# Kernel tuning notes

Hardware: AMD Instinct MI355X
Metric: run time of the kernel (lower is better)

## Reference

```python
import jax, jax.numpy as jnp
import numpy as np

GROUP = 128  # per-group quantization along the input dimension


def _quantize_int4(w):
    """Asymmetric INT4 per-group quantization. w: [out, in] -> (q, scale, zero).
    q: int32 in [0,15], shape [out, in//GROUP, GROUP]; scale/zero: [out, in//GROUP]."""
    o, i = w.shape
    wg = w.reshape(o, i // GROUP, GROUP)
    mn = wg.min(axis=-1)
    mx = wg.max(axis=-1)
    scale = (mx - mn) / 15.0
    scale = jnp.where(scale == 0, jnp.float32(1.0), scale)
    zero = jnp.clip(jnp.round(-mn / scale), 0.0, 15.0)
    q = jnp.clip(jnp.round(wg / scale[..., None]) + zero[..., None], 0.0, 15.0).astype(jnp.int32)
    return q, scale.astype(jnp.float32), zero.astype(jnp.float32)


def _dequant(q, s, z):
    """(q - zero) * scale, regrouped back to [out, in]."""
    w = (q.astype(jnp.float32) - z[..., None]) * s[..., None]
    return w.reshape(q.shape[0], -1)


def setup_inputs() -> dict:
    key = jax.random.key(0)
    ks = jax.random.split(key, 5)
    B, D_IN, D_H, D_OUT = 512, 2048, 8192, 2048
    x = jax.random.normal(ks[0], (B, D_IN), dtype=jnp.float32)
    w1 = jax.random.normal(ks[1], (D_H, D_IN), dtype=jnp.float32) * 0.02
    b1 = jax.random.normal(ks[2], (D_H,), dtype=jnp.float32) * 0.01
    w2 = jax.random.normal(ks[3], (D_OUT, D_H), dtype=jnp.float32) * 0.02
    b2 = jax.random.normal(ks[4], (D_OUT,), dtype=jnp.float32) * 0.01
    q1, s1, z1 = _quantize_int4(w1)
    q2, s2, z2 = _quantize_int4(w2)
    return {"x": x, "q1": q1, "s1": s1, "z1": z1, "b1": b1,
            "q2": q2, "s2": s2, "z2": z2, "b2": b2}


def reference(x, q1, s1, z1, b1, q2, s2, z2, b2):
    # Layer 1: INT4 dequant + Linear + ReLU (fused in the native kernel)
    w1 = _dequant(q1, s1, z1)              # [D_H, D_IN]
    h = jax.nn.relu(x @ w1.T + b1)         # [B, D_H]
    # Layer 2: INT4 dequant + Linear (no activation)
    w2 = _dequant(q2, s2, z2)              # [D_OUT, D_H]
    return h @ w2.T + b2                   # [B, D_OUT]
```

## Files before the change

kernel.cpp:

```cpp
#include <hip/hip_runtime.h>
#include <stdint.h>

typedef unsigned short u16;
typedef _Float16 f16;
typedef __attribute__((ext_vector_type(8))) _Float16 f16x8;
typedef __attribute__((ext_vector_type(4))) float f32x4;
typedef __attribute__((ext_vector_type(4))) int i32x4;

#define LW 56
#define LWI 28

#define BARRIER() asm volatile("s_waitcnt lgkmcnt(0)\n\ts_barrier" ::: "memory")

__device__ __forceinline__ int pk2(float a, float b) {
  return __builtin_bit_cast(int, __builtin_amdgcn_cvt_pkrtz(a, b));
}


__global__ __launch_bounds__(256) void cvt_x(const float* __restrict__ src,
                                             i32x4* __restrict__ dst, int n8) {
  int t = blockIdx.x * 256 + threadIdx.x;
  if (t >= n8) return;
  f32x4 a = ((const f32x4*)src)[2 * t];
  f32x4 b = ((const f32x4*)src)[2 * t + 1];
  i32x4 o = {pk2(a[0], a[1]), pk2(a[2], a[3]), pk2(b[0], b[1]), pk2(b[2], b[3])};
  dst[t] = o;
}

__global__ __launch_bounds__(256) void bias_init(float* __restrict__ out,
                                                 const float* __restrict__ b, int n4) {
  int t = blockIdx.x * 256 + threadIdx.x;
  if (t >= n4) return;
  int idx = t * 4;
  *(f32x4*)(out + idx) = *(const f32x4*)(b + (idx & 2047));
}

__global__ __launch_bounds__(256, 2) void gemm1(const u16* __restrict__ X,
                                                const int* __restrict__ Q,
                                                const float* __restrict__ S,
                                                const float* __restrict__ Z,
                                                const float* __restrict__ bias,
                                                f16* __restrict__ H) {
  const int K = 2048, N = 8192, G = 16;
  __shared__ int As[2][64 * LWI];
  __shared__ int Bs[2][128 * LWI];
  const int tid = threadIdx.x;
  const int wave = tid >> 6, lane = tid & 63, quad = lane >> 4, l15 = lane & 15;
  const int m0 = blockIdx.y << 6, n0 = blockIdx.x << 7;
  const int wm = (wave >> 1) << 5, wn = (wave & 1) << 6;
  const int arow = tid >> 2, ak = (tid & 3) << 3;
  const int brow = tid >> 1, bk = (tid & 1) << 4;

  const u16* ap = X + (size_t)(m0 + arow) * K + ak;
  const int* qp = Q + (size_t)(n0 + brow) * K + bk;
  const float* sp = S + (n0 + brow) * G;
  const float* zp = Z + (n0 + brow) * G;

  i32x4 nq0 = *(const i32x4*)(qp);
  i32x4 nq1 = *(const i32x4*)(qp + 4);
  i32x4 nq2 = *(const i32x4*)(qp + 8);
  i32x4 nq3 = *(const i32x4*)(qp + 12);
  i32x4 na = *(const i32x4*)(ap);
  float ns = sp[0], nz = zp[0];

  f32x4 acc[2][4];
#pragma unroll
  for (int i = 0; i < 2; i++)
#pragma unroll
    for (int j = 0; j < 4; j++) acc[i][j] = (f32x4){0.f, 0.f, 0.f, 0.f};

#pragma unroll 2
  for (int k = 0; k < K; k += 32) {
    const int buf = (k >> 5) & 1;
    i32x4 q0 = nq0, q1 = nq1, q2 = nq2, q3 = nq3, av = na;
    const float f = ns, o = -nz * ns;
    if (k + 32 < K) {
      nq0 = *(const i32x4*)(qp + k + 32);
      nq1 = *(const i32x4*)(qp + k + 36);
      nq2 = *(const i32x4*)(qp + k + 40);
      nq3 = *(const i32x4*)(qp + k + 44);
      na = *(const i32x4*)(ap + k + 32);
      const int g = (k + 32) >> 7;
      ns = sp[g];
      nz = zp[g];
    }
    i32x4 lo = {pk2(fmaf((float)q0[0], f, o), fmaf((float)q0[1], f, o)),
                pk2(fmaf((float)q0[2], f, o), fmaf((float)q0[3], f, o)),
                pk2(fmaf((float)q1[0], f, o), fmaf((float)q1[1], f, o)),
                pk2(fmaf((float)q1[2], f, o), fmaf((float)q1[3], f, o))};
    i32x4 hi = {pk2(fmaf((float)q2[0], f, o), fmaf((float)q2[1], f, o)),
                pk2(fmaf((float)q2[2], f, o), fmaf((float)q2[3], f, o)),
                pk2(fmaf((float)q3[0], f, o), fmaf((float)q3[1], f, o)),
                pk2(fmaf((float)q3[2], f, o), fmaf((float)q3[3], f, o))};
    *(i32x4*)&Bs[buf][brow * LWI + (bk >> 1)] = lo;
    *(i32x4*)&Bs[buf][brow * LWI + (bk >> 1) + 4] = hi;
    *(i32x4*)&As[buf][arow * LWI + (ak >> 1)] = av;
    BARRIER();
    const f16* AsH = (const f16*)As[buf];
    const f16* BsH = (const f16*)Bs[buf];
    f16x8 af[2], bf[4];
#pragma unroll
    for (int i = 0; i < 2; i++)
      af[i] = *(const f16x8*)&AsH[(wm + i * 16 + l15) * LW + quad * 8];
#pragma unroll
    for (int j = 0; j < 4; j++)
      bf[j] = *(const f16x8*)&BsH[(wn + j * 16 + l15) * LW + quad * 8];
#pragma unroll
    for (int i = 0; i < 2; i++)
#pragma unroll
      for (int j = 0; j < 4; j++)
        acc[i][j] = __builtin_amdgcn_mfma_f32_16x16x32_f16(af[i], bf[j], acc[i][j], 0, 0, 0);
  }

#pragma unroll
  for (int i = 0; i < 2; i++)
#pragma unroll
    for (int j = 0; j < 4; j++) {
      const int col = n0 + wn + j * 16 + l15;
      const float bv = bias[col];
#pragma unroll
      for (int r = 0; r < 4; r++) {
        const int row = m0 + wm + i * 16 + quad * 4 + r;
        float v = acc[i][j][r] + bv;
        v = v > 0.f ? v : 0.f;
        H[(size_t)row * N + col] = (f16)v;
      }
    }
}

__global__ __launch_bounds__(256, 2) void gemm2(const u16* __restrict__ Hm,
                                                const int* __restrict__ Q,
                                                const float* __restrict__ S,
                                                const float* __restrict__ Z,
                                                float* __restrict__ out) {
  const int K = 8192, N = 2048, G = 64, KCH = 1024;
  __shared__ int As[2][128 * LWI];
  __shared__ int Bs[2][128 * LWI];
  const int tid = threadIdx.x;
  const int wave = tid >> 6, lane = tid & 63, quad = lane >> 4, l15 = lane & 15;
  const int m0 = blockIdx.y << 7, n0 = blockIdx.x << 7;
  const int kStart = blockIdx.z << 10;
  const int wm = (wave >> 1) << 6, wn = (wave & 1) << 6;
  const int arow = tid >> 1, ak = (tid & 1) << 4;
  const int brow = tid >> 1, bk = (tid & 1) << 4;

  const u16* ap = Hm + (size_t)(m0 + arow) * K + kStart + ak;
  const int* qp = Q + (size_t)(n0 + brow) * K + kStart + bk;
  const float* sp = S + (n0 + brow) * G;
  const float* zp = Z + (n0 + brow) * G;
  const int g0 = kStart >> 7;

  i32x4 nq0 = *(const i32x4*)(qp);
  i32x4 nq1 = *(const i32x4*)(qp + 4);
  i32x4 nq2 = *(const i32x4*)(qp + 8);
  i32x4 nq3 = *(const i32x4*)(qp + 12);
  i32x4 na0 = *(const i32x4*)(ap);
  i32x4 na1 = *(const i32x4*)(ap + 8);
  float ns = sp[g0], nz = zp[g0];

  f32x4 acc[4][4];
#pragma unroll
  for (int i = 0; i < 4; i++)
#pragma unroll
    for (int j = 0; j < 4; j++) acc[i][j] = (f32x4){0.f, 0.f, 0.f, 0.f};

#pragma unroll 2
  for (int k = 0; k < KCH; k += 32) {
    const int buf = (k >> 5) & 1;
    i32x4 q0 = nq0, q1 = nq1, q2 = nq2, q3 = nq3, a0 = na0, a1 = na1;
    const float f = ns, o = -nz * ns;
    if (k + 32 < KCH) {
      nq0 = *(const i32x4*)(qp + k + 32);
      nq1 = *(const i32x4*)(qp + k + 36);
      nq2 = *(const i32x4*)(qp + k + 40);
      nq3 = *(const i32x4*)(qp + k + 44);
      na0 = *(const i32x4*)(ap + k + 32);
      na1 = *(const i32x4*)(ap + k + 40);
      const int g = (kStart + k + 32) >> 7;
      ns = sp[g];
      nz = zp[g];
    }
    i32x4 lo = {pk2(fmaf((float)q0[0], f, o), fmaf((float)q0[1], f, o)),
                pk2(fmaf((float)q0[2], f, o), fmaf((float)q0[3], f, o)),
                pk2(fmaf((float)q1[0], f, o), fmaf((float)q1[1], f, o)),
                pk2(fmaf((float)q1[2], f, o), fmaf((float)q1[3], f, o))};
    i32x4 hi = {pk2(fmaf((float)q2[0], f, o), fmaf((float)q2[1], f, o)),
                pk2(fmaf((float)q2[2], f, o), fmaf((float)q2[3], f, o)),
                pk2(fmaf((float)q3[0], f, o), fmaf((float)q3[1], f, o)),
                pk2(fmaf((float)q3[2], f, o), fmaf((float)q3[3], f, o))};
    *(i32x4*)&Bs[buf][brow * LWI + (bk >> 1)] = lo;
    *(i32x4*)&Bs[buf][brow * LWI + (bk >> 1) + 4] = hi;
    *(i32x4*)&As[buf][arow * LWI + (ak >> 1)] = a0;
    *(i32x4*)&As[buf][arow * LWI + (ak >> 1) + 4] = a1;
    BARRIER();
    const f16* AsH = (const f16*)As[buf];
    const f16* BsH = (const f16*)Bs[buf];
    f16x8 af[4], bf[4];
#pragma unroll
    for (int i = 0; i < 4; i++)
      af[i] = *(const f16x8*)&AsH[(wm + i * 16 + l15) * LW + quad * 8];
#pragma unroll
    for (int j = 0; j < 4; j++)
      bf[j] = *(const f16x8*)&BsH[(wn + j * 16 + l15) * LW + quad * 8];
#pragma unroll
    for (int i = 0; i < 4; i++)
#pragma unroll
      for (int j = 0; j < 4; j++)
        acc[i][j] = __builtin_amdgcn_mfma_f32_16x16x32_f16(af[i], bf[j], acc[i][j], 0, 0, 0);
  }

#pragma unroll
  for (int i = 0; i < 4; i++)
#pragma unroll
    for (int j = 0; j < 4; j++) {
      const int col = n0 + wn + j * 16 + l15;
#pragma unroll
      for (int r = 0; r < 4; r++) {
        const int row = m0 + wm + i * 16 + quad * 4 + r;
        atomicAdd(out + (size_t)row * N + col, acc[i][j][r]);
      }
    }
}


extern "C" void kernel_launch(void* const* d_in, const int* in_sizes, int n_in,
                              void* d_out, int out_size, void* d_ws, size_t ws_size,
                              hipStream_t stream) {
  const float* x = (const float*)d_in[0];
  const int* q1 = (const int*)d_in[1];
  const float* s1 = (const float*)d_in[2];
  const float* z1 = (const float*)d_in[3];
  const float* b1 = (const float*)d_in[4];
  const int* q2 = (const int*)d_in[5];
  const float* s2 = (const float*)d_in[6];
  const float* z2 = (const float*)d_in[7];
  const float* b2 = (const float*)d_in[8];
  float* out = (float*)d_out;

  const int B = 512, D_IN = 2048, D_H = 8192, D_OUT = 2048;

  char* ws = (char*)d_ws;
  u16* xh = (u16*)ws;
  u16* h = (u16*)(ws + (size_t)2 * 1024 * 1024);

  cvt_x<<<(B * D_IN / 8 + 255) / 256, 256, 0, stream>>>(x, (i32x4*)xh, B * D_IN / 8);
  bias_init<<<(B * D_OUT / 4 + 255) / 256, 256, 0, stream>>>(out, b2, B * D_OUT / 4);

  dim3 g1(D_H / 128, B / 64, 1);
  gemm1<<<g1, 256, 0, stream>>>(xh, q1, s1, z1, b1, (f16*)h);

  dim3 g2(D_OUT / 128, B / 128, 8);
  gemm2<<<g2, 256, 0, stream>>>(h, q2, s2, z2, out);
}
```

Before: 291.1 us.

## Drop LDS staging, dequantize INT4 in registers with f16 magic-number trick

Both GEMMs stop staging tiles through shared memory and barriers. Each lane now loads its MFMA fragments straight from global memory and dequantizes weights in packed f16 using the 0x6400 exponent trick. gemm1 moves to 128x128 tiles and also writes the b2 bias into out, which removes the bias_init launch. gemm2 switches to split-K of 4 with longer K chunks. The aim is to cut LDS traffic, barriers, fp32 conversion work and one kernel launch, at the cost of redundant global loads across waves, fewer blocks in flight, and f16 rounding of scale and zero.

```diff
diff --git a/kernel.cpp b/kernel.cpp
--- a/kernel.cpp
+++ b/kernel.cpp
@@ -3,19 +3,28 @@
 
 typedef unsigned short u16;
 typedef _Float16 f16;
+typedef __attribute__((ext_vector_type(2))) _Float16 f16x2;
 typedef __attribute__((ext_vector_type(8))) _Float16 f16x8;
 typedef __attribute__((ext_vector_type(4))) float f32x4;
 typedef __attribute__((ext_vector_type(4))) int i32x4;
 
-#define LW 56
-#define LWI 28
-
-#define BARRIER() asm volatile("s_waitcnt lgkmcnt(0)\n\ts_barrier" ::: "memory")
-
 __device__ __forceinline__ int pk2(float a, float b) {
   return __builtin_bit_cast(int, __builtin_amdgcn_cvt_pkrtz(a, b));
 }
 
+__device__ __forceinline__ f16x8 dq8(i32x4 qa, i32x4 qb, f16x2 z2, f16x2 s2) {
+  unsigned u0 = (unsigned)qa[0] | ((unsigned)qa[1] << 16) | 0x64006400u;
+  unsigned u1 = (unsigned)qa[2] | ((unsigned)qa[3] << 16) | 0x64006400u;
+  unsigned u2 = (unsigned)qb[0] | ((unsigned)qb[1] << 16) | 0x64006400u;
+  unsigned u3 = (unsigned)qb[2] | ((unsigned)qb[3] << 16) | 0x64006400u;
+  f16x2 w0 = (__builtin_bit_cast(f16x2, u0) - z2) * s2;
+  f16x2 w1 = (__builtin_bit_cast(f16x2, u1) - z2) * s2;
+  f16x2 w2 = (__builtin_bit_cast(f16x2, u2) - z2) * s2;
+  f16x2 w3 = (__builtin_bit_cast(f16x2, u3) - z2) * s2;
+  i32x4 t = {__builtin_bit_cast(int, w0), __builtin_bit_cast(int, w1),
+             __builtin_bit_cast(int, w2), __builtin_bit_cast(int, w3)};
+  return __builtin_bit_cast(f16x8, t);
+}
 
 __global__ __launch_bounds__(256) void cvt_x(const float* __restrict__ src,
                                              i32x4* __restrict__ dst, int n8) {
@@ -27,97 +36,96 @@
   dst[t] = o;
 }
 
-__global__ __launch_bounds__(256) void bias_init(float* __restrict__ out,
-                                                 const float* __restrict__ b, int n4) {
-  int t = blockIdx.x * 256 + threadIdx.x;
-  if (t >= n4) return;
-  int idx = t * 4;
-  *(f32x4*)(out + idx) = *(const f32x4*)(b + (idx & 2047));
-}
-
-__global__ __launch_bounds__(256, 2) void gemm1(const u16* __restrict__ X,
-                                                const int* __restrict__ Q,
-                                                const float* __restrict__ S,
-                                                const float* __restrict__ Z,
-                                                const float* __restrict__ bias,
-                                                f16* __restrict__ H) {
+__global__ __launch_bounds__(256) void gemm1(const f16* __restrict__ X,
+                                             const int* __restrict__ Q,
+                                             const float* __restrict__ S,
+                                             const float* __restrict__ Z,
+                                             const float* __restrict__ b1,
+                                             const float* __restrict__ b2,
+                                             f16* __restrict__ H,
+                                             float* __restrict__ out) {
   const int K = 2048, N = 8192, G = 16;
-  __shared__ int As[2][64 * LWI];
-  __shared__ int Bs[2][128 * LWI];
-  const int tid = threadIdx.x;
-  const int wave = tid >> 6, lane = tid & 63, quad = lane >> 4, l15 = lane & 15;
-  const int m0 = blockIdx.y << 6, n0 = blockIdx.x << 7;
-  const int wm = (wave >> 1) << 5, wn = (wave & 1) << 6;
-  const int arow = tid >> 2, ak = (tid & 3) << 3;
-  const int brow = tid >> 1, bk = (tid & 1) << 4;
-
-  const u16* ap = X + (size_t)(m0 + arow) * K + ak;
-  const int* qp = Q + (size_t)(n0 + brow) * K + bk;
-  const float* sp = S + (n0 + brow) * G;
-  const float* zp = Z + (n0 + brow) * G;
-
-  i32x4 nq0 = *(const i32x4*)(qp);
-  i32x4 nq1 = *(const i32x4*)(qp + 4);
-  i32x4 nq2 = *(const i32x4*)(qp + 8);
-  i32x4 nq3 = *(const i32x4*)(qp + 12);
-  i32x4 na = *(const i32x4*)(ap);
-  float ns = sp[0], nz = zp[0];
-
-  f32x4 acc[2][4];
-#pragma unroll
-  for (int i = 0; i < 2; i++)
+  const int tid = threadIdx.x, wave = tid >> 6, lane = tid & 63;
+  const int quad = lane >> 4, l15 = lane & 15;
+  const int m0 = blockIdx.y << 7, n0 = blockIdx.x << 7;
+  const int wm = (wave >> 1) << 6, wn = (wave & 1) << 6;
+
+  const f16* aP[4];
+  const int* qP[4];
+  int nrow[4];
+#pragma unroll
+  for (int i = 0; i < 4; i++) aP[i] = X + (size_t)(m0 + wm + i * 16 + l15) * K + quad * 8;
+#pragma unroll
+  for (int j = 0; j < 4; j++) {
+    nrow[j] = n0 + wn + j * 16 + l15;
+    qP[j] = Q + (size_t)nrow[j] * K + quad * 8;
+  }
+
+  i32x4 qa[4], qb[4];
+  f16x8 af[4];
+  f16x2 s2[4], z2[4];
+#pragma unroll
+  for (int j = 0; j < 4; j++) {
+    qa[j] = *(const i32x4*)(qP[j]);
+    qb[j] = *(const i32x4*)(qP[j] + 4);
+    float s = S[nrow[j] * G], z = Z[nrow[j] * G];
+    f16 sh = (f16)s, zh = (f16)(1024.f + z);
+    s2[j] = (f16x2){sh, sh};
+    z2[j] = (f16x2){zh, zh};
+  }
+#pragma unroll
+  for (int i = 0; i < 4; i++) af[i] = *(const f16x8*)(aP[i]);
+
+  f32x4 acc[4][4];
+#pragma unroll
+  for (int i = 0; i < 4; i++)
 #pragma unroll
     for (int j = 0; j < 4; j++) acc[i][j] = (f32x4){0.f, 0.f, 0.f, 0.f};
 
 #pragma unroll 2
   for (int k = 0; k < K; k += 32) {
-    const int buf = (k >> 5) & 1;
-    i32x4 q0 = nq0, q1 = nq1, q2 = nq2, q3 = nq3, av = na;
-    const float f = ns, o = -nz * ns;
+    i32x4 cqa[4], cqb[4];
+    f16x8 caf[4];
+    f16x2 cs2[4], cz2[4];
+#pragma unroll
+    for (int j = 0; j < 4; j++) { cqa[j] = qa[j]; cqb[j] = qb[j]; cs2[j] = s2[j]; cz2[j] = z2[j]; }
+#pragma unroll
+    for (int i = 0; i < 4; i++) caf[i] = af[i];
     if (k + 32 < K) {
-      nq0 = *(const i32x4*)(qp + k + 32);
-      nq1 = *(const i32x4*)(qp + k + 36);
-      nq2 = *(const i32x4*)(qp + k + 40);
-      nq3 = *(const i32x4*)(qp + k + 44);
-      na = *(const i32x4*)(ap + k + 32);
-      const int g = (k + 32) >> 7;
-      ns = sp[g];
-      nz = zp[g];
-    }
-    i32x4 lo = {pk2(fmaf((float)q0[0], f, o), fmaf((float)q0[1], f, o)),
-                pk2(fmaf((float)q0[2], f, o), fmaf((float)q0[3], f, o)),
-                pk2(fmaf((float)q1[0], f, o), fmaf((float)q1[1], f, o)),
-                pk2(fmaf((float)q1[2], f, o), fmaf((float)q1[3], f, o))};
-    i32x4 hi = {pk2(fmaf((float)q2[0], f, o), fmaf((float)q2[1], f, o)),
-                pk2(fmaf((float)q2[2], f, o), fmaf((float)q2[3], f, o)),
-                pk2(fmaf((float)q3[0], f, o), fmaf((float)q3[1], f, o)),
-                pk2(fmaf((float)q3[2], f, o), fmaf((float)q3[3], f, o))};
-    *(i32x4*)&Bs[buf][brow * LWI + (bk >> 1)] = lo;
-    *(i32x4*)&Bs[buf][brow * LWI + (bk >> 1) + 4] = hi;
-    *(i32x4*)&As[buf][arow * LWI + (ak >> 1)] = av;
-    BARRIER();
-    const f16* AsH = (const f16*)As[buf];
-    const f16* BsH = (const f16*)Bs[buf];
-    f16x8 af[2], bf[4];
-#pragma unroll
-    for (int i = 0; i < 2; i++)
-      af[i] = *(const f16x8*)&AsH[(wm + i * 16 + l15) * LW + quad * 8];
-#pragma unroll
-    for (int j = 0; j < 4; j++)
-      bf[j] = *(const f16x8*)&BsH[(wn + j * 16 + l15) * LW + quad * 8];
-#pragma unroll
-    for (int i = 0; i < 2; i++)
+#pragma unroll
+      for (int j = 0; j < 4; j++) {
+        qa[j] = *(const i32x4*)(qP[j] + k + 32);
+        qb[j] = *(const i32x4*)(qP[j] + k + 36);
+      }
+#pragma unroll
+      for (int i = 0; i < 4; i++) af[i] = *(const f16x8*)(aP[i] + k + 32);
+      if (((k + 32) & 127) == 0) {
+        const int g = (k + 32) >> 7;
+#pragma unroll
+        for (int j = 0; j < 4; j++) {
+          float s = S[nrow[j] * G + g], z = Z[nrow[j] * G + g];
+          f16 sh = (f16)s, zh = (f16)(1024.f + z);
+          s2[j] = (f16x2){sh, sh};
+          z2[j] = (f16x2){zh, zh};
+        }
+      }
+    }
+    f16x8 bf[4];
+#pragma unroll
+    for (int j = 0; j < 4; j++) bf[j] = dq8(cqa[j], cqb[j], cz2[j], cs2[j]);
+#pragma unroll
+    for (int i = 0; i < 4; i++)
 #pragma unroll
       for (int j = 0; j < 4; j++)
-        acc[i][j] = __builtin_amdgcn_mfma_f32_16x16x32_f16(af[i], bf[j], acc[i][j], 0, 0, 0);
-  }
-
-#pragma unroll
-  for (int i = 0; i < 2; i++)
+        acc[i][j] = __builtin_amdgcn_mfma_f32_16x16x32_f16(caf[i], bf[j], acc[i][j], 0, 0, 0);
+  }
+
+#pragma unroll
+  for (int i = 0; i < 4; i++)
 #pragma unroll
     for (int j = 0; j < 4; j++) {
       const int col = n0 + wn + j * 16 + l15;
-      const float bv = bias[col];
+      const float bv = b1[col];
 #pragma unroll
       for (int r = 0; r < 4; r++) {
         const int row = m0 + wm + i * 16 + quad * 4 + r;
@@ -126,37 +134,57 @@
         H[(size_t)row * N + col] = (f16)v;
       }
     }
-}
-
-__global__ __launch_bounds__(256, 2) void gemm2(const u16* __restrict__ Hm,
-                                                const int* __restrict__ Q,
-                                                const float* __restrict__ S,
-                                                const float* __restrict__ Z,
-                                                float* __restrict__ out) {
-  const int K = 8192, N = 2048, G = 64, KCH = 1024;
-  __shared__ int As[2][128 * LWI];
-  __shared__ int Bs[2][128 * LWI];
-  const int tid = threadIdx.x;
-  const int wave = tid >> 6, lane = tid & 63, quad = lane >> 4, l15 = lane & 15;
+
+  {
+    const int lin = (int)(blockIdx.y * gridDim.x + blockIdx.x);
+    const int base = lin * 4096 + tid * 16;
+#pragma unroll
+    for (int e = 0; e < 4; e++) {
+      const int idx = base + e * 4;
+      *(f32x4*)(out + idx) = *(const f32x4*)(b2 + (idx & 2047));
+    }
+  }
+}
+
+__global__ __launch_bounds__(256) void gemm2(const f16* __restrict__ Hm,
+                                             const int* __restrict__ Q,
+                                             const float* __restrict__ S,
+                                             const float* __restrict__ Z,
+                                             float* __restrict__ out) {
+  const int K = 8192, N = 2048, G = 64, KCH = 2048;
+  const int tid = threadIdx.x, wave = tid >> 6, lane = tid & 63;
+  const int quad = lane >> 4, l15 = lane & 15;
   const int m0 = blockIdx.y << 7, n0 = blockIdx.x << 7;
-  const int kStart = blockIdx.z << 10;
+  const int kStart = blockIdx.z << 11;
   const int wm = (wave >> 1) << 6, wn = (wave & 1) << 6;
-  const int arow = tid >> 1, ak = (tid & 1) << 4;
-  const int brow = tid >> 1, bk = (tid & 1) << 4;
-
-  const u16* ap = Hm + (size_t)(m0 + arow) * K + kStart + ak;
-  const int* qp = Q + (size_t)(n0 + brow) * K + kStart + bk;
-  const float* sp = S + (n0 + brow) * G;
-  const float* zp = Z + (n0 + brow) * G;
+
+  const f16* aP[4];
+  const int* qP[4];
+  int nrow[4];
+#pragma unroll
+  for (int i = 0; i < 4; i++)
+    aP[i] = Hm + (size_t)(m0 + wm + i * 16 + l15) * K + kStart + quad * 8;
+#pragma unroll
+  for (int j = 0; j < 4; j++) {
+    nrow[j] = n0 + wn + j * 16 + l15;
+    qP[j] = Q + (size_t)nrow[j] * K + kStart + quad * 8;
+  }
+
+  i32x4 qa[4], qb[4];
+  f16x8 af[4];
+  f16x2 s2[4], z2[4];
   const int g0 = kStart >> 7;
-
-  i32x4 nq0 = *(const i32x4*)(qp);
-  i32x4 nq1 = *(const i32x4*)(qp + 4);
-  i32x4 nq2 = *(const i32x4*)(qp + 8);
-  i32x4 nq3 = *(const i32x4*)(qp + 12);
-  i32x4 na0 = *(const i32x4*)(ap);
-  i32x4 na1 = *(const i32x4*)(ap + 8);
-  float ns = sp[g0], nz = zp[g0];
+#pragma unroll
+  for (int j = 0; j < 4; j++) {
+    qa[j] = *(const i32x4*)(qP[j]);
+    qb[j] = *(const i32x4*)(qP[j] + 4);
+    float s = S[nrow[j] * G + g0], z = Z[nrow[j] * G + g0];
+    f16 sh = (f16)s, zh = (f16)(1024.f + z);
+    s2[j] = (f16x2){sh, sh};
+    z2[j] = (f16x2){zh, zh};
+  }
+#pragma unroll
+  for (int i = 0; i < 4; i++) af[i] = *(const f16x8*)(aP[i]);
 
   f32x4 acc[4][4];
 #pragma unroll
@@ -166,47 +194,40 @@
 
 #pragma unroll 2
   for (int k = 0; k < KCH; k += 32) {
-    const int buf = (k >> 5) & 1;
-    i32x4 q0 = nq0, q1 = nq1, q2 = nq2, q3 = nq3, a0 = na0, a1 = na1;
-    const float f = ns, o = -nz * ns;
+    i32x4 cqa[4], cqb[4];
+    f16x8 caf[4];
+    f16x2 cs2[4], cz2[4];
+#pragma unroll
+    for (int j = 0; j < 4; j++) { cqa[j] = qa[j]; cqb[j] = qb[j]; cs2[j] = s2[j]; cz2[j] = z2[j]; }
+#pragma unroll
+    for (int i = 0; i < 4; i++) caf[i] = af[i];
     if (k + 32 < KCH) {
-      nq0 = *(const i32x4*)(qp + k + 32);
-      nq1 = *(const i32x4*)(qp + k + 36);
-      nq2 = *(const i32x4*)(qp + k + 40);
-      nq3 = *(const i32x4*)(qp + k + 44);
-      na0 = *(const i32x4*)(ap + k + 32);
-      na1 = *(const i32x4*)(ap + k + 40);
-      const int g = (kStart + k + 32) >> 7;
-      ns = sp[g];
-      nz = zp[g];
-    }
-    i32x4 lo = {pk2(fmaf((float)q0[0], f, o), fmaf((float)q0[1], f, o)),
-                pk2(fmaf((float)q0[2], f, o), fmaf((float)q0[3], f, o)),
-                pk2(fmaf((float)q1[0], f, o), fmaf((float)q1[1], f, o)),
-                pk2(fmaf((float)q1[2], f, o), fmaf((float)q1[3], f, o))};
-    i32x4 hi = {pk2(fmaf((float)q2[0], f, o), fmaf((float)q2[1], f, o)),
-                pk2(fmaf((float)q2[2], f, o), fmaf((float)q2[3], f, o)),
-                pk2(fmaf((float)q3[0], f, o), fmaf((float)q3[1], f, o)),
-                pk2(fmaf((float)q3[2], f, o), fmaf((float)q3[3], f, o))};
-    *(i32x4*)&Bs[buf][brow * LWI + (bk >> 1)] = lo;
-    *(i32x4*)&Bs[buf][brow * LWI + (bk >> 1) + 4] = hi;
-    *(i32x4*)&As[buf][arow * LWI + (ak >> 1)] = a0;
-    *(i32x4*)&As[buf][arow * LWI + (ak >> 1) + 4] = a1;
-    BARRIER();
-    const f16* AsH = (const f16*)As[buf];
-    const f16* BsH = (const f16*)Bs[buf];
-    f16x8 af[4], bf[4];
+#pragma unroll
+      for (int j = 0; j < 4; j++) {
+        qa[j] = *(const i32x4*)(qP[j] + k + 32);
+        qb[j] = *(const i32x4*)(qP[j] + k + 36);
+      }
+#pragma unroll
+      for (int i = 0; i < 4; i++) af[i] = *(const f16x8*)(aP[i] + k + 32);
+      if (((k + 32) & 127) == 0) {
+        const int g = (kStart + k + 32) >> 7;
+#pragma unroll
+        for (int j = 0; j < 4; j++) {
+          float s = S[nrow[j] * G + g], z = Z[nrow[j] * G + g];
+          f16 sh = (f16)s, zh = (f16)(1024.f + z);
+          s2[j] = (f16x2){sh, sh};
+          z2[j] = (f16x2){zh, zh};
+        }
+      }
+    }
+    f16x8 bf[4];
+#pragma unroll
+    for (int j = 0; j < 4; j++) bf[j] = dq8(cqa[j], cqb[j], cz2[j], cs2[j]);
 #pragma unroll
     for (int i = 0; i < 4; i++)
-      af[i] = *(const f16x8*)&AsH[(wm + i * 16 + l15) * LW + quad * 8];
-#pragma unroll
-    for (int j = 0; j < 4; j++)
-      bf[j] = *(const f16x8*)&BsH[(wn + j * 16 + l15) * LW + quad * 8];
-#pragma unroll
-    for (int i = 0; i < 4; i++)
 #pragma unroll
       for (int j = 0; j < 4; j++)
-        acc[i][j] = __builtin_amdgcn_mfma_f32_16x16x32_f16(af[i], bf[j], acc[i][j], 0, 0, 0);
+        acc[i][j] = __builtin_amdgcn_mfma_f32_16x16x32_f16(caf[i], bf[j], acc[i][j], 0, 0, 0);
   }
 
 #pragma unroll
@@ -221,7 +242,6 @@
       }
     }
 }
-
 
 extern "C" void kernel_launch(void* const* d_in, const int* in_sizes, int n_in,
                               void* d_out, int out_size, void* d_ws, size_t ws_size,
@@ -237,18 +257,11 @@
   const float* b2 = (const float*)d_in[8];
   float* out = (float*)d_out;
 
-  const int B = 512, D_IN = 2048, D_H = 8192, D_OUT = 2048;
-
   char* ws = (char*)d_ws;
-  u16* xh = (u16*)ws;
-  u16* h = (u16*)(ws + (size_t)2 * 1024 * 1024);
-
-  cvt_x<<<(B * D_IN / 8 + 255) / 256, 256, 0, stream>>>(x, (i32x4*)xh, B * D_IN / 8);
-  bias_init<<<(B * D_OUT / 4 + 255) / 256, 256, 0, stream>>>(out, b2, B * D_OUT / 4);
-
-  dim3 g1(D_H / 128, B / 64, 1);
-  gemm1<<<g1, 256, 0, stream>>>(xh, q1, s1, z1, b1, (f16*)h);
-
-  dim3 g2(D_OUT / 128, B / 128, 8);
-  gemm2<<<g2, 256, 0, stream>>>(h, q2, s2, z2, out);
-}
+  f16* xh = (f16*)ws;
+  f16* h = (f16*)(ws + (size_t)2 * 1024 * 1024);
+
+  cvt_x<<<512, 256, 0, stream>>>(x, (i32x4*)xh, 512 * 2048 / 8);
+  gemm1<<<dim3(64, 4), 256, 0, stream>>>(xh, q1, s1, z1, b1, b2, h, out);
+  gemm2<<<dim3(16, 4, 4), 256, 0, stream>>>(h, q2, s2, z2, out);
+}
```

New measurement: 342.0 us. +17.5%, slower.

## Use direct global-to-LDS loads, f16 magic-number dequant, fused prep kernel

Applied to the files above, without the earlier changes.

Activation tiles are now loaded straight into shared memory with global_load_lds using an XOR-swizzled layout, and no longer pass through registers. INT4 weights are dequantized in packed f16 math with the 0x6400 magic-number trick, replacing per-element float convert and FMA. The x conversion and bias init kernels are merged into one launch, and grids are flattened to 1D with a new block ordering. Doing the dequant arithmetic in f16 rather than f32 may change accuracy, and the vmcnt drain each iteration could serialize loads.

```diff
diff --git a/kernel.cpp b/kernel.cpp
--- a/kernel.cpp
+++ b/kernel.cpp
@@ -3,64 +3,86 @@
 
 typedef unsigned short u16;
 typedef _Float16 f16;
+typedef __attribute__((ext_vector_type(2))) _Float16 f16x2;
 typedef __attribute__((ext_vector_type(8))) _Float16 f16x8;
 typedef __attribute__((ext_vector_type(4))) float f32x4;
 typedef __attribute__((ext_vector_type(4))) int i32x4;
 
-#define LW 56
-#define LWI 28
-
-#define BARRIER() asm volatile("s_waitcnt lgkmcnt(0)\n\ts_barrier" ::: "memory")
+#define BSTRIDE 40
+
+#define GLD16(g, l)                                                         \
+  __builtin_amdgcn_global_load_lds(                                         \
+      (const __attribute__((address_space(1))) void*)(g),                   \
+      (__attribute__((address_space(3))) void*)(l), 16, 0, 0)
+
+#define DRAIN_VM() asm volatile("s_waitcnt vmcnt(0)" ::: "memory")
+#define BARRIER_LGKM() asm volatile("s_waitcnt lgkmcnt(0)\n\ts_barrier" ::: "memory")
 
 __device__ __forceinline__ int pk2(float a, float b) {
   return __builtin_bit_cast(int, __builtin_amdgcn_cvt_pkrtz(a, b));
 }
 
-
-__global__ __launch_bounds__(256) void cvt_x(const float* __restrict__ src,
-                                             i32x4* __restrict__ dst, int n8) {
-  int t = blockIdx.x * 256 + threadIdx.x;
-  if (t >= n8) return;
-  f32x4 a = ((const f32x4*)src)[2 * t];
-  f32x4 b = ((const f32x4*)src)[2 * t + 1];
+__device__ __forceinline__ f16x8 dq8(i32x4 qa, i32x4 qb, f16x2 z2, f16x2 s2) {
+  unsigned u0 = (unsigned)qa[0] | ((unsigned)qa[1] << 16) | 0x64006400u;
+  unsigned u1 = (unsigned)qa[2] | ((unsigned)qa[3] << 16) | 0x64006400u;
+  unsigned u2 = (unsigned)qb[0] | ((unsigned)qb[1] << 16) | 0x64006400u;
+  unsigned u3 = (unsigned)qb[2] | ((unsigned)qb[3] << 16) | 0x64006400u;
+  f16x2 w0 = (__builtin_bit_cast(f16x2, u0) - z2) * s2;
+  f16x2 w1 = (__builtin_bit_cast(f16x2, u1) - z2) * s2;
+  f16x2 w2 = (__builtin_bit_cast(f16x2, u2) - z2) * s2;
+  f16x2 w3 = (__builtin_bit_cast(f16x2, u3) - z2) * s2;
+  i32x4 t = {__builtin_bit_cast(int, w0), __builtin_bit_cast(int, w1),
+             __builtin_bit_cast(int, w2), __builtin_bit_cast(int, w3)};
+  return __builtin_bit_cast(f16x8, t);
+}
+
+__global__ __launch_bounds__(256) void cvt_init(const float* __restrict__ x,
+                                                const float* __restrict__ b2,
+                                                f16* __restrict__ xh,
+                                                float* __restrict__ out) {
+  const int g = blockIdx.x * 256 + threadIdx.x;
+  f32x4 a = ((const f32x4*)x)[2 * g];
+  f32x4 b = ((const f32x4*)x)[2 * g + 1];
   i32x4 o = {pk2(a[0], a[1]), pk2(a[2], a[3]), pk2(b[0], b[1]), pk2(b[2], b[3])};
-  dst[t] = o;
-}
-
-__global__ __launch_bounds__(256) void bias_init(float* __restrict__ out,
-                                                 const float* __restrict__ b, int n4) {
-  int t = blockIdx.x * 256 + threadIdx.x;
-  if (t >= n4) return;
-  int idx = t * 4;
-  *(f32x4*)(out + idx) = *(const f32x4*)(b + (idx & 2047));
-}
-
-__global__ __launch_bounds__(256, 2) void gemm1(const u16* __restrict__ X,
-                                                const int* __restrict__ Q,
-                                                const float* __restrict__ S,
-                                                const float* __restrict__ Z,
-                                                const float* __restrict__ bias,
-                                                f16* __restrict__ H) {
-  const int K = 2048, N = 8192, G = 16;
-  __shared__ int As[2][64 * LWI];
-  __shared__ int Bs[2][128 * LWI];
-  const int tid = threadIdx.x;
+  ((i32x4*)xh)[g] = o;
+  const int oi = g * 8;
+  *(f32x4*)(out + oi) = *(const f32x4*)(b2 + (oi & 2047));
+  *(f32x4*)(out + oi + 4) = *(const f32x4*)(b2 + ((oi + 4) & 2047));
+}
+
+__global__ __launch_bounds__(256, 2) void gemm1_k(const f16* __restrict__ X,
+                                                  const int* __restrict__ Q,
+                                                  const float* __restrict__ S,
+                                                  const float* __restrict__ Z,
+                                                  const float* __restrict__ b1,
+                                                  f16* __restrict__ H) {
+  __shared__ char smem[36864];
+  f16* As0 = (f16*)smem;
+  f16* As1 = (f16*)(smem + 8192);
+  f16* Bs0 = (f16*)(smem + 16384);
+  f16* Bs1 = (f16*)(smem + 16384 + 10240);
+  const int tid = threadIdx.x, bid = blockIdx.x;
   const int wave = tid >> 6, lane = tid & 63, quad = lane >> 4, l15 = lane & 15;
-  const int m0 = blockIdx.y << 6, n0 = blockIdx.x << 7;
+  const int K = 2048, G = 16;
+  const int mt = bid >> 6, nt = bid & 63;
+  const int m0 = mt << 6, n0 = nt << 7;
   const int wm = (wave >> 1) << 5, wn = (wave & 1) << 6;
-  const int arow = tid >> 2, ak = (tid & 3) << 3;
-  const int brow = tid >> 1, bk = (tid & 1) << 4;
-
-  const u16* ap = X + (size_t)(m0 + arow) * K + ak;
-  const int* qp = Q + (size_t)(n0 + brow) * K + bk;
-  const float* sp = S + (n0 + brow) * G;
-  const float* zp = Z + (n0 + brow) * G;
-
-  i32x4 nq0 = *(const i32x4*)(qp);
-  i32x4 nq1 = *(const i32x4*)(qp + 4);
-  i32x4 nq2 = *(const i32x4*)(qp + 8);
-  i32x4 nq3 = *(const i32x4*)(qp + 12);
-  i32x4 na = *(const i32x4*)(ap);
+
+  const int sr = lane >> 2, sc = (lane & 3) ^ (sr & 3);
+  const f16* asrc = X + (size_t)(m0 + 16 * wave + sr) * K + sc * 8;
+  const int adoff = wave * 1024;
+
+  const int brow = tid >> 1, bhf = tid & 1;
+  const int grow = n0 + brow;
+  const int* qp = Q + (size_t)grow * K + bhf * 16;
+  const float* sp = S + grow * G;
+  const float* zp = Z + grow * G;
+
+  GLD16(asrc, (char*)As0 + adoff);
+  i32x4 nb0 = *(const i32x4*)(qp);
+  i32x4 nb1 = *(const i32x4*)(qp + 4);
+  i32x4 nb2 = *(const i32x4*)(qp + 8);
+  i32x4 nb3 = *(const i32x4*)(qp + 12);
   float ns = sp[0], nz = zp[0];
 
   f32x4 acc[2][4];
@@ -72,39 +94,36 @@
 #pragma unroll 2
   for (int k = 0; k < K; k += 32) {
     const int buf = (k >> 5) & 1;
-    i32x4 q0 = nq0, q1 = nq1, q2 = nq2, q3 = nq3, av = na;
-    const float f = ns, o = -nz * ns;
+    f16* AsB = buf ? As1 : As0;
+    f16* BsB = buf ? Bs1 : Bs0;
+    DRAIN_VM();
+    i32x4 c0 = nb0, c1 = nb1, c2 = nb2, c3 = nb3;
+    const f16 sh = (f16)ns, zh = (f16)(1024.f + nz);
+    const f16x2 s2v = {sh, sh}, z2v = {zh, zh};
+    f16x8 w0 = dq8(c0, c1, z2v, s2v);
+    f16x8 w1 = dq8(c2, c3, z2v, s2v);
+    *(f16x8*)&BsB[brow * BSTRIDE + bhf * 16] = w0;
+    *(f16x8*)&BsB[brow * BSTRIDE + bhf * 16 + 8] = w1;
+    BARRIER_LGKM();
+    f16x8 af[2], bf[4];
+#pragma unroll
+    for (int i = 0; i < 2; i++) {
+      const int R = wm + i * 16 + l15;
+      af[i] = *(const f16x8*)&AsB[R * 32 + ((quad ^ (R & 3)) << 3)];
+    }
+#pragma unroll
+    for (int j = 0; j < 4; j++)
+      bf[j] = *(const f16x8*)&BsB[(wn + j * 16 + l15) * BSTRIDE + quad * 8];
     if (k + 32 < K) {
-      nq0 = *(const i32x4*)(qp + k + 32);
-      nq1 = *(const i32x4*)(qp + k + 36);
-      nq2 = *(const i32x4*)(qp + k + 40);
-      nq3 = *(const i32x4*)(qp + k + 44);
-      na = *(const i32x4*)(ap + k + 32);
+      GLD16(asrc + k + 32, (char*)(buf ? As0 : As1) + adoff);
+      nb0 = *(const i32x4*)(qp + k + 32);
+      nb1 = *(const i32x4*)(qp + k + 36);
+      nb2 = *(const i32x4*)(qp + k + 40);
+      nb3 = *(const i32x4*)(qp + k + 44);
       const int g = (k + 32) >> 7;
       ns = sp[g];
       nz = zp[g];
     }
-    i32x4 lo = {pk2(fmaf((float)q0[0], f, o), fmaf((float)q0[1], f, o)),
-                pk2(fmaf((float)q0[2], f, o), fmaf((float)q0[3], f, o)),
-                pk2(fmaf((float)q1[0], f, o), fmaf((float)q1[1], f, o)),
-                pk2(fmaf((float)q1[2], f, o), fmaf((float)q1[3], f, o))};
-    i32x4 hi = {pk2(fmaf((float)q2[0], f, o), fmaf((float)q2[1], f, o)),
-                pk2(fmaf((float)q2[2], f, o), fmaf((float)q2[3], f, o)),
-                pk2(fmaf((float)q3[0], f, o), fmaf((float)q3[1], f, o)),
-                pk2(fmaf((float)q3[2], f, o), fmaf((float)q3[3], f, o))};
-    *(i32x4*)&Bs[buf][brow * LWI + (bk >> 1)] = lo;
-    *(i32x4*)&Bs[buf][brow * LWI + (bk >> 1) + 4] = hi;
-    *(i32x4*)&As[buf][arow * LWI + (ak >> 1)] = av;
-    BARRIER();
-    const f16* AsH = (const f16*)As[buf];
-    const f16* BsH = (const f16*)Bs[buf];
-    f16x8 af[2], bf[4];
-#pragma unroll
-    for (int i = 0; i < 2; i++)
-      af[i] = *(const f16x8*)&AsH[(wm + i * 16 + l15) * LW + quad * 8];
-#pragma unroll
-    for (int j = 0; j < 4; j++)
-      bf[j] = *(const f16x8*)&BsH[(wn + j * 16 + l15) * LW + quad * 8];
 #pragma unroll
     for (int i = 0; i < 2; i++)
 #pragma unroll
@@ -117,46 +136,53 @@
 #pragma unroll
     for (int j = 0; j < 4; j++) {
       const int col = n0 + wn + j * 16 + l15;
-      const float bv = bias[col];
+      const float bv = b1[col];
 #pragma unroll
       for (int r = 0; r < 4; r++) {
         const int row = m0 + wm + i * 16 + quad * 4 + r;
         float v = acc[i][j][r] + bv;
         v = v > 0.f ? v : 0.f;
-        H[(size_t)row * N + col] = (f16)v;
+        H[(size_t)row * 8192 + col] = (f16)v;
       }
     }
 }
 
-__global__ __launch_bounds__(256, 2) void gemm2(const u16* __restrict__ Hm,
-                                                const int* __restrict__ Q,
-                                                const float* __restrict__ S,
-                                                const float* __restrict__ Z,
-                                                float* __restrict__ out) {
-  const int K = 8192, N = 2048, G = 64, KCH = 1024;
-  __shared__ int As[2][128 * LWI];
-  __shared__ int Bs[2][128 * LWI];
-  const int tid = threadIdx.x;
+__global__ __launch_bounds__(256, 2) void gemm2_k(const f16* __restrict__ Hm,
+                                                  const int* __restrict__ Q,
+                                                  const float* __restrict__ S,
+                                                  const float* __restrict__ Z,
+                                                  float* __restrict__ out) {
+  __shared__ char smem[36864];
+  f16* As0 = (f16*)smem;
+  f16* As1 = (f16*)(smem + 8192);
+  f16* Bs0 = (f16*)(smem + 16384);
+  f16* Bs1 = (f16*)(smem + 16384 + 10240);
+  const int tid = threadIdx.x, bid = blockIdx.x;
   const int wave = tid >> 6, lane = tid & 63, quad = lane >> 4, l15 = lane & 15;
-  const int m0 = blockIdx.y << 7, n0 = blockIdx.x << 7;
-  const int kStart = blockIdx.z << 10;
+  const int K = 8192, G = 64;
+  const int zb = bid & 7, nt = (bid >> 3) & 15, mt = bid >> 7;
+  const int m0 = mt << 7, n0 = nt << 7;
+  const int kStart = zb << 10;
   const int wm = (wave >> 1) << 6, wn = (wave & 1) << 6;
-  const int arow = tid >> 1, ak = (tid & 1) << 4;
-  const int brow = tid >> 1, bk = (tid & 1) << 4;
-
-  const u16* ap = Hm + (size_t)(m0 + arow) * K + kStart + ak;
-  const int* qp = Q + (size_t)(n0 + brow) * K + kStart + bk;
-  const float* sp = S + (n0 + brow) * G;
-  const float* zp = Z + (n0 + brow) * G;
-  const int g0 = kStart >> 7;
-
-  i32x4 nq0 = *(const i32x4*)(qp);
-  i32x4 nq1 = *(const i32x4*)(qp + 4);
-  i32x4 nq2 = *(const i32x4*)(qp + 8);
-  i32x4 nq3 = *(const i32x4*)(qp + 12);
-  i32x4 na0 = *(const i32x4*)(ap);
-  i32x4 na1 = *(const i32x4*)(ap + 8);
-  float ns = sp[g0], nz = zp[g0];
+
+  const int sr = lane >> 2, sc = (lane & 3) ^ (sr & 3);
+  const f16* asrc = Hm + (size_t)(m0 + 32 * wave + sr) * K + kStart + sc * 8;
+  const size_t arow16 = (size_t)16 * K;
+  const int adoff = wave * 2048;
+
+  const int brow = tid >> 1, bhf = tid & 1;
+  const int grow = n0 + brow;
+  const int* qp = Q + (size_t)grow * K + kStart + bhf * 16;
+  const float* sp = S + grow * G;
+  const float* zp = Z + grow * G;
+
+  GLD16(asrc, (char*)As0 + adoff);
+  GLD16(asrc + arow16, (char*)As0 + adoff + 1024);
+  i32x4 nb0 = *(const i32x4*)(qp);
+  i32x4 nb1 = *(const i32x4*)(qp + 4);
+  i32x4 nb2 = *(const i32x4*)(qp + 8);
+  i32x4 nb3 = *(const i32x4*)(qp + 12);
+  float ns = sp[kStart >> 7], nz = zp[kStart >> 7];
 
   f32x4 acc[4][4];
 #pragma unroll
@@ -165,43 +191,40 @@
     for (int j = 0; j < 4; j++) acc[i][j] = (f32x4){0.f, 0.f, 0.f, 0.f};
 
 #pragma unroll 2
-  for (int k = 0; k < KCH; k += 32) {
+  for (int k = 0; k < 1024; k += 32) {
     const int buf = (k >> 5) & 1;
-    i32x4 q0 = nq0, q1 = nq1, q2 = nq2, q3 = nq3, a0 = na0, a1 = na1;
-    const float f = ns, o = -nz * ns;
-    if (k + 32 < KCH) {
-      nq0 = *(const i32x4*)(qp + k + 32);
-      nq1 = *(const i32x4*)(qp + k + 36);
-      nq2 = *(const i32x4*)(qp + k + 40);
-      nq3 = *(const i32x4*)(qp + k + 44);
-      na0 = *(const i32x4*)(ap + k + 32);
-      na1 = *(const i32x4*)(ap + k + 40);
+    f16* AsB = buf ? As1 : As0;
+    f16* BsB = buf ? Bs1 : Bs0;
+    DRAIN_VM();
+    i32x4 c0 = nb0, c1 = nb1, c2 = nb2, c3 = nb3;
+    const f16 sh = (f16)ns, zh = (f16)(1024.f + nz);
+    const f16x2 s2v = {sh, sh}, z2v = {zh, zh};
+    f16x8 w0 = dq8(c0, c1, z2v, s2v);
+    f16x8 w1 = dq8(c2, c3, z2v, s2v);
+    *(f16x8*)&BsB[brow * BSTRIDE + bhf * 16] = w0;
+    *(f16x8*)&BsB[brow * BSTRIDE + bhf * 16 + 8] = w1;
+    BARRIER_LGKM();
+    f16x8 af[4], bf[4];
+#pragma unroll
+    for (int i = 0; i < 4; i++) {
+      const int R = wm + i * 16 + l15;
+      af[i] = *(const f16x8*)&AsB[R * 32 + ((quad ^ (R & 3)) << 3)];
+    }
+#pragma unroll
+    for (int j = 0; j < 4; j++)
+      bf[j] = *(const f16x8*)&BsB[(wn + j * 16 + l15) * BSTRIDE + quad * 8];
+    if (k + 32 < 1024) {
+      char* AsN = (char*)(buf ? As0 : As1);
+      GLD16(asrc + k + 32, AsN + adoff);
+      GLD16(asrc + k + 32 + arow16, AsN + adoff + 1024);
+      nb0 = *(const i32x4*)(qp + k + 32);
+      nb1 = *(const i32x4*)(qp + k + 36);
+      nb2 = *(const i32x4*)(qp + k + 40);
+      nb3 = *(const i32x4*)(qp + k + 44);
       const int g = (kStart + k + 32) >> 7;
       ns = sp[g];
       nz = zp[g];
     }
-    i32x4 lo = {pk2(fmaf((float)q0[0], f, o), fmaf((float)q0[1], f, o)),
-                pk2(fmaf((float)q0[2], f, o), fmaf((float)q0[3], f, o)),
-                pk2(fmaf((float)q1[0], f, o), fmaf((float)q1[1], f, o)),
-                pk2(fmaf((float)q1[2], f, o), fmaf((float)q1[3], f, o))};
-    i32x4 hi = {pk2(fmaf((float)q2[0], f, o), fmaf((float)q2[1], f, o)),
-                pk2(fmaf((float)q2[2], f, o), fmaf((float)q2[3], f, o)),
-                pk2(fmaf((float)q3[0], f, o), fmaf((float)q3[1], f, o)),
-                pk2(fmaf((float)q3[2], f, o), fmaf((float)q3[3], f, o))};
-    *(i32x4*)&Bs[buf][brow * LWI + (bk >> 1)] = lo;
-    *(i32x4*)&Bs[buf][brow * LWI + (bk >> 1) + 4] = hi;
-    *(i32x4*)&As[buf][arow * LWI + (ak >> 1)] = a0;
-    *(i32x4*)&As[buf][arow * LWI + (ak >> 1) + 4] = a1;
-    BARRIER();
-    const f16* AsH = (const f16*)As[buf];
-    const f16* BsH = (const f16*)Bs[buf];
-    f16x8 af[4], bf[4];
-#pragma unroll
-    for (int i = 0; i < 4; i++)
-      af[i] = *(const f16x8*)&AsH[(wm + i * 16 + l15) * LW + quad * 8];
-#pragma unroll
-    for (int j = 0; j < 4; j++)
-      bf[j] = *(const f16x8*)&BsH[(wn + j * 16 + l15) * LW + quad * 8];
 #pragma unroll
     for (int i = 0; i < 4; i++)
 #pragma unroll
@@ -217,11 +240,10 @@
 #pragma unroll
       for (int r = 0; r < 4; r++) {
         const int row = m0 + wm + i * 16 + quad * 4 + r;
-        atomicAdd(out + (size_t)row * N + col, acc[i][j][r]);
+        atomicAdd(out + (size_t)row * 2048 + col, acc[i][j][r]);
       }
     }
 }
-
 
 extern "C" void kernel_launch(void* const* d_in, const int* in_sizes, int n_in,
                               void* d_out, int out_size, void* d_ws, size_t ws_size,
@@ -237,18 +259,11 @@
   const float* b2 = (const float*)d_in[8];
   float* out = (float*)d_out;
 
-  const int B = 512, D_IN = 2048, D_H = 8192, D_OUT = 2048;
-
   char* ws = (char*)d_ws;
-  u16* xh = (u16*)ws;
-  u16* h = (u16*)(ws + (size_t)2 * 1024 * 1024);
-
-  cvt_x<<<(B * D_IN / 8 + 255) / 256, 256, 0, stream>>>(x, (i32x4*)xh, B * D_IN / 8);
-  bias_init<<<(B * D_OUT / 4 + 255) / 256, 256, 0, stream>>>(out, b2, B * D_OUT / 4);
-
-  dim3 g1(D_H / 128, B / 64, 1);
-  gemm1<<<g1, 256, 0, stream>>>(xh, q1, s1, z1, b1, (f16*)h);
-
-  dim3 g2(D_OUT / 128, B / 128, 8);
-  gemm2<<<g2, 256, 0, stream>>>(h, q2, s2, z2, out);
-}
+  f16* xh = (f16*)ws;
+  f16* h = (f16*)(ws + (size_t)2 * 1024 * 1024);
+
+  cvt_init<<<512, 256, 0, stream>>>(x, b2, xh, out);
+  gemm1_k<<<512, 256, 0, stream>>>(xh, q1, s1, z1, b1, h);
+  gemm2_k<<<512, 256, 0, stream>>>(h, q2, s2, z2, out);
+}
```

Result: no change. 290.7 us (-0.2%).
